# Optimization experiments

Hardware: AMD Instinct MI355X
Metric: run time of the kernel (lower is better)

## Reference

```python
import jax, jax.numpy as jnp
import numpy as np


def setup_inputs() -> dict:
    key = jax.random.key(0)
    k1, k2, k3 = jax.random.split(key, 3)
    B, T, D, H = 64, 512, 1024, 1024
    x = jax.random.normal(k1, (B, T, D), dtype=jnp.float32)
    state = jnp.zeros((B, H), dtype=jnp.float32)
    W = jax.random.normal(k2, (H, H), dtype=jnp.float32) / np.sqrt(H).astype(np.float32)
    U = jax.random.normal(k3, (D, H), dtype=jnp.float32) / np.sqrt(D).astype(np.float32)
    b = jnp.zeros((H,), dtype=jnp.float32)
    return {"x": x, "state": state, "W": W, "U": U, "b": b}


def reference(x, state, W, U, b):
    # x: (B, T, D) -> precompute input projection for all steps: (T, B, H)
    xU = jnp.einsum('btd,dh->tbh', x, U) + b

    def step(h, xu_t):
        h = jnp.tanh(xu_t + h @ W)
        return h, h

    final_state, outs = jax.lax.scan(step, state, xU)  # outs: (T, B, H)
    outs = jnp.transpose(outs, (1, 0, 2))  # (B, T, H)
    return outs, final_state
```

## Files before the change

kernel.cpp:

```cpp
#include <hip/hip_runtime.h>
#include <hip/hip_fp16.h>

typedef float  f4v __attribute__((ext_vector_type(4)));
typedef _Float16 h8v __attribute__((ext_vector_type(8)));
typedef _Float16 h4v __attribute__((ext_vector_type(4)));

#define B_ 64
#define T_ 512
#define H_ 1024

__global__ __launch_bounds__(256) void k_transpose_cvt(const float* __restrict__ src,
                                                       _Float16* __restrict__ dst) {
  __shared__ _Float16 tile[64][72];
  int r0 = blockIdx.y * 64, c0 = blockIdx.x * 64;
  int t = threadIdx.x;
  for (int i = 0; i < 4; ++i) {
    int r = i * 16 + (t >> 4);
    int c = (t & 15) * 4;
    f4v v = *reinterpret_cast<const f4v*>(src + (long)(r0 + r) * 1024 + c0 + c);
    tile[c + 0][r] = (_Float16)v.x;
    tile[c + 1][r] = (_Float16)v.y;
    tile[c + 2][r] = (_Float16)v.z;
    tile[c + 3][r] = (_Float16)v.w;
  }
  __syncthreads();
  for (int i = 0; i < 2; ++i) {
    int rr = i * 32 + (t >> 3);
    int cc = (t & 7) * 8;
    *reinterpret_cast<h8v*>(dst + (long)(c0 + rr) * 1024 + r0 + cc) =
        *reinterpret_cast<const h8v*>(&tile[rr][cc]);
  }
}

#define SWZG(r, kh) ((((r) * 64) + ((kh) * 2)) ^ (((r) & 3) << 4))

__global__ __launch_bounds__(256) void k_gemm_xu(const float* __restrict__ x,
                                                 const _Float16* __restrict__ Ut,
                                                 const float* __restrict__ bias,
                                                 float* __restrict__ out) {
  __shared__ __attribute__((aligned(16))) unsigned char Asm[128 * 32 * 2];
  __shared__ __attribute__((aligned(16))) unsigned char Bsm[128 * 32 * 2];
  int bid = blockIdx.x;
  int nt = bid & 7, mt = bid >> 3;
  int t = threadIdx.x;
  int row = t >> 1, kc = (t & 1) * 16;
  long gA = (long)(mt * 128 + row) * 1024 + kc;
  long gB = (long)(nt * 128 + row) * 1024 + kc;
  int wid = t >> 6, lane = t & 63;
  int wr = (wid >> 1) * 64, wc = (wid & 1) * 64;
  int l15 = lane & 15, khi = (lane >> 4) * 8;

  f4v acc[4][4];
  for (int i = 0; i < 4; ++i)
    for (int j = 0; j < 4; ++j) acc[i][j] = (f4v){0.f, 0.f, 0.f, 0.f};

  f4v ra[4];
  h8v rb[2];
  {
    const float* ap = x + gA;
    ra[0] = *(const f4v*)(ap);     ra[1] = *(const f4v*)(ap + 4);
    ra[2] = *(const f4v*)(ap + 8); ra[3] = *(const f4v*)(ap + 12);
    const _Float16* bp = Ut + gB;
    rb[0] = *(const h8v*)(bp);     rb[1] = *(const h8v*)(bp + 8);
  }
  for (int kt = 0; kt < 32; ++kt) {
    h8v ah0, ah1;
    for (int j = 0; j < 4; ++j) {
      ah0[j]     = (_Float16)ra[0][j];
      ah0[j + 4] = (_Float16)ra[1][j];
      ah1[j]     = (_Float16)ra[2][j];
      ah1[j + 4] = (_Float16)ra[3][j];
    }
    *(h8v*)(Asm + SWZG(row, kc))     = ah0;
    *(h8v*)(Asm + SWZG(row, kc + 8)) = ah1;
    *(h8v*)(Bsm + SWZG(row, kc))     = rb[0];
    *(h8v*)(Bsm + SWZG(row, kc + 8)) = rb[1];
    __syncthreads();
    if (kt < 31) {
      const float* ap = x + gA + (kt + 1) * 32;
      ra[0] = *(const f4v*)(ap);     ra[1] = *(const f4v*)(ap + 4);
      ra[2] = *(const f4v*)(ap + 8); ra[3] = *(const f4v*)(ap + 12);
      const _Float16* bp = Ut + gB + (kt + 1) * 32;
      rb[0] = *(const h8v*)(bp);     rb[1] = *(const h8v*)(bp + 8);
    }
    h8v af[4], bf[4];
    for (int mi = 0; mi < 4; ++mi)
      af[mi] = *(const h8v*)(Asm + SWZG(wr + mi * 16 + l15, khi));
    for (int ni = 0; ni < 4; ++ni)
      bf[ni] = *(const h8v*)(Bsm + SWZG(wc + ni * 16 + l15, khi));
    for (int mi = 0; mi < 4; ++mi)
      for (int ni = 0; ni < 4; ++ni)
        acc[mi][ni] = __builtin_amdgcn_mfma_f32_16x16x32_f16(af[mi], bf[ni], acc[mi][ni], 0, 0, 0);
    __syncthreads();
  }
  int coff = nt * 128 + wc, roff = mt * 128 + wr;
  for (int ni = 0; ni < 4; ++ni) {
    int col = coff + ni * 16 + l15;
    float bb = bias[col];
    for (int mi = 0; mi < 4; ++mi) {
      int rbase = roff + mi * 16 + (lane >> 4) * 4;
      for (int j = 0; j < 4; ++j)
        out[(long)(rbase + j) * 1024 + col] = acc[mi][ni][j] + bb;
    }
  }
}

#define SWZS(r, kh) ((((r) * 2048) + ((kh) * 2)) ^ (((r) & 7) << 4))

__global__ __launch_bounds__(256) void k_scan(const float* __restrict__ state,
                                              float* __restrict__ out,
                                              const _Float16* __restrict__ Wt,
                                              unsigned int* __restrict__ ctr) {
  extern __shared__ __attribute__((aligned(16))) unsigned char smem[];
  unsigned char* Wl = smem;
  unsigned char* Hl = smem + 65536;
  int t = threadIdx.x;
  int cl = blockIdx.x & 7;
  int mm = blockIdx.x >> 3;

  {
    int r = t >> 3, c8 = t & 7;
    const _Float16* wsrc = Wt + (long)(mm * 32 + r) * 1024;
    for (int j = 0; j < 16; ++j) {
      int kh = (c8 + 8 * j) * 8;
      *(h8v*)(Wl + SWZS(r, kh)) = *(const h8v*)(wsrc + kh);
    }
  }

  unsigned int* myctr = ctr + cl * 64;
  int wid = t >> 6, lane = t & 63;
  int srow = t >> 5, slane = t & 31;
  long b = cl * 8 + srow;
  int l15 = lane & 15, khi8 = (lane >> 4) * 8;
  int arow = lane & 7;
  int bro = wid * 16 + l15;
  int hi = lane >> 4;
  int gcol = mm * 32 + wid * 16 + l15;

  for (int step = 0; step < T_; ++step) {
    const float* hsrc = (step == 0) ? (state + b * 1024)
                                    : (out + (b * T_ + (step - 1)) * 1024);
    const float* hp = hsrc + slane * 4;
    f4v w0, w1, w2, w3, w4, w5, w6, w7;
    asm volatile(
        "global_load_dwordx4 %0, %8, off sc0 sc1\n\t"
        "global_load_dwordx4 %1, %8, off offset:512 sc0 sc1\n\t"
        "global_load_dwordx4 %2, %8, off offset:1024 sc0 sc1\n\t"
        "global_load_dwordx4 %3, %8, off offset:1536 sc0 sc1\n\t"
        "global_load_dwordx4 %4, %8, off offset:2048 sc0 sc1\n\t"
        "global_load_dwordx4 %5, %8, off offset:2560 sc0 sc1\n\t"
        "global_load_dwordx4 %6, %8, off offset:3072 sc0 sc1\n\t"
        "global_load_dwordx4 %7, %8, off offset:3584 sc0 sc1\n\t"
        "s_waitcnt vmcnt(0)"
        : "=&v"(w0), "=&v"(w1), "=&v"(w2), "=&v"(w3),
          "=&v"(w4), "=&v"(w5), "=&v"(w6), "=&v"(w7)
        : "v"(hp)
        : "memory");
    {
      f4v wv[8] = {w0, w1, w2, w3, w4, w5, w6, w7};
#pragma unroll
      for (int j = 0; j < 8; ++j) {
        int k = (slane + 32 * j) * 4;
        h4v hv;
        hv[0] = (_Float16)wv[j][0]; hv[1] = (_Float16)wv[j][1];
        hv[2] = (_Float16)wv[j][2]; hv[3] = (_Float16)wv[j][3];
        *(h4v*)(Hl + SWZS(srow, k)) = hv;
      }
    }
    __syncthreads();

    if (wid < 2) {
      float xuv[4];
      long addr0 = 0;
      if (hi < 2) {
        addr0 = ((long)(cl * 8 + hi * 4) * T_ + step) * 1024 + gcol;
#pragma unroll
        for (int j = 0; j < 4; ++j) xuv[j] = out[addr0 + (long)j * T_ * 1024];
      }
      f4v acc0 = (f4v){0.f, 0.f, 0.f, 0.f}, acc1 = acc0;
#pragma unroll
      for (int s = 0; s < 32; s += 2) {
        int k0 = s * 32 + khi8, k1 = (s + 1) * 32 + khi8;
        h8v af0 = *(const h8v*)(Hl + SWZS(arow, k0));
        h8v bf0 = *(const h8v*)(Wl + SWZS(bro, k0));
        h8v af1 = *(const h8v*)(Hl + SWZS(arow, k1));
        h8v bf1 = *(const h8v*)(Wl + SWZS(bro, k1));
        acc0 = __builtin_amdgcn_mfma_f32_16x16x32_f16(af0, bf0, acc0, 0, 0, 0);
        acc1 = __builtin_amdgcn_mfma_f32_16x16x32_f16(af1, bf1, acc1, 0, 0, 0);
      }
      f4v acc = acc0 + acc1;
      if (hi < 2) {
        float v0 = tanhf(acc[0] + xuv[0]);
        float v1 = tanhf(acc[1] + xuv[1]);
        float v2 = tanhf(acc[2] + xuv[2]);
        float v3 = tanhf(acc[3] + xuv[3]);
        float* p0 = out + addr0;
        float* p1 = p0 + (long)T_ * 1024;
        float* p2 = p1 + (long)T_ * 1024;
        float* p3 = p2 + (long)T_ * 1024;
        asm volatile(
            "global_store_dword %0, %4, off sc0 sc1\n\t"
            "global_store_dword %1, %5, off sc0 sc1\n\t"
            "global_store_dword %2, %6, off sc0 sc1\n\t"
            "global_store_dword %3, %7, off sc0 sc1\n\t"
            "s_waitcnt vmcnt(0)"
            :: "v"(p0), "v"(p1), "v"(p2), "v"(p3),
               "v"(v0), "v"(v1), "v"(v2), "v"(v3)
            : "memory");
        if (step == T_ - 1) {
          long r = (long)cl * 8 + hi * 4;
          float* q = out + (long)B_ * T_ * 1024 + r * 1024 + gcol;
          q[0] = v0; q[1024] = v1; q[2048] = v2; q[3072] = v3;
        }
      }
    }

    __syncthreads();
    if (t == 0) {
      __hip_atomic_fetch_add(myctr, 1u, __ATOMIC_RELAXED, __HIP_MEMORY_SCOPE_AGENT);
      unsigned int tgt = 32u * (unsigned)(step + 1);
      while (__hip_atomic_load(myctr, __ATOMIC_RELAXED, __HIP_MEMORY_SCOPE_AGENT) < tgt)
        __builtin_amdgcn_s_sleep(1);
    }
    __syncthreads();
  }
}

extern "C" void kernel_launch(void* const* d_in, const int* in_sizes, int n_in,
                              void* d_out, int out_size, void* d_ws, size_t ws_size,
                              hipStream_t stream) {
  const float* x     = (const float*)d_in[0];
  const float* state = (const float*)d_in[1];
  const float* W     = (const float*)d_in[2];
  const float* U     = (const float*)d_in[3];
  const float* bias  = (const float*)d_in[4];
  float* out = (float*)d_out;
  unsigned char* ws = (unsigned char*)d_ws;

  _Float16* Ut = (_Float16*)ws;
  _Float16* Wt = (_Float16*)(ws + (1u << 21));
  unsigned int* ctr = (unsigned int*)(ws + (1u << 22));

  hipMemsetAsync(ctr, 0, 8 * 64 * sizeof(unsigned int), stream);

  k_transpose_cvt<<<dim3(16, 16), 256, 0, stream>>>(U, Ut);
  k_transpose_cvt<<<dim3(16, 16), 256, 0, stream>>>(W, Wt);
  k_gemm_xu<<<2048, 256, 0, stream>>>(x, Ut, bias, out);

  hipFuncSetAttribute((const void*)k_scan, hipFuncAttributeMaxDynamicSharedMemorySize, 81920);
  void* args[] = {(void*)&state, (void*)&out, (void*)&Wt, (void*)&ctr};
  hipLaunchCooperativeKernel((void*)k_scan, dim3(256), dim3(256), args, 81920, stream);
}
```

Measured before the change: 1.602 ms.

## Replace counter barrier with step-tagged fp16 hidden-state exchange buffer

Removes the per-step atomic counter barrier and its two block-wide syncs. Each block now publishes the new hidden state as fp16 values packed with a 16-bit step tag into a double-buffered exchange array, and consumers spin-load until every tag matches the expected step. The shared-memory H buffer is double-buffered and the MFMA loop uses four accumulators instead of two. The exchange buffer reuses the Ut workspace after the projection GEMM and is reset with a 0xFF memset. Correctness depends on tag polling and cross-block visibility of the stores, and rows that arrive late are re-polled in full.

```diff
diff --git a/kernel.cpp b/kernel.cpp
--- a/kernel.cpp
+++ b/kernel.cpp
@@ -4,6 +4,7 @@
 typedef float  f4v __attribute__((ext_vector_type(4)));
 typedef _Float16 h8v __attribute__((ext_vector_type(8)));
 typedef _Float16 h4v __attribute__((ext_vector_type(4)));
+typedef unsigned uv4 __attribute__((ext_vector_type(4)));
 
 #define B_ 64
 #define T_ 512
@@ -107,16 +108,30 @@
 
 #define SWZS(r, kh) ((((r) * 2048) + ((kh) * 2)) ^ (((r) & 7) << 4))
 
+static __device__ __forceinline__ _Float16 lo_h(unsigned u) {
+  unsigned short s = (unsigned short)u;
+  _Float16 h;
+  __builtin_memcpy(&h, &s, 2);
+  return h;
+}
+static __device__ __forceinline__ unsigned pk(float f, unsigned tg) {
+  _Float16 h = (_Float16)f;
+  unsigned short s;
+  __builtin_memcpy(&s, &h, 2);
+  return (tg << 16) | (unsigned)s;
+}
+
 __global__ __launch_bounds__(256) void k_scan(const float* __restrict__ state,
                                               float* __restrict__ out,
                                               const _Float16* __restrict__ Wt,
-                                              unsigned int* __restrict__ ctr) {
+                                              unsigned* __restrict__ hx) {
   extern __shared__ __attribute__((aligned(16))) unsigned char smem[];
   unsigned char* Wl = smem;
-  unsigned char* Hl = smem + 65536;
+  unsigned char* Hl0 = smem + 65536;
   int t = threadIdx.x;
-  int cl = blockIdx.x & 7;
-  int mm = blockIdx.x >> 3;
+  int bid = blockIdx.x;
+  int cl = bid & 7;
+  int mm = bid >> 3;
 
   {
     int r = t >> 3, c8 = t & 7;
@@ -127,7 +142,6 @@
     }
   }
 
-  unsigned int* myctr = ctr + cl * 64;
   int wid = t >> 6, lane = t & 63;
   int srow = t >> 5, slane = t & 31;
   long b = cl * 8 + srow;
@@ -138,33 +152,64 @@
   int gcol = mm * 32 + wid * 16 + l15;
 
   for (int step = 0; step < T_; ++step) {
-    const float* hsrc = (step == 0) ? (state + b * 1024)
-                                    : (out + (b * T_ + (step - 1)) * 1024);
-    const float* hp = hsrc + slane * 4;
-    f4v w0, w1, w2, w3, w4, w5, w6, w7;
-    asm volatile(
-        "global_load_dwordx4 %0, %8, off sc0 sc1\n\t"
-        "global_load_dwordx4 %1, %8, off offset:512 sc0 sc1\n\t"
-        "global_load_dwordx4 %2, %8, off offset:1024 sc0 sc1\n\t"
-        "global_load_dwordx4 %3, %8, off offset:1536 sc0 sc1\n\t"
-        "global_load_dwordx4 %4, %8, off offset:2048 sc0 sc1\n\t"
-        "global_load_dwordx4 %5, %8, off offset:2560 sc0 sc1\n\t"
-        "global_load_dwordx4 %6, %8, off offset:3072 sc0 sc1\n\t"
-        "global_load_dwordx4 %7, %8, off offset:3584 sc0 sc1\n\t"
-        "s_waitcnt vmcnt(0)"
-        : "=&v"(w0), "=&v"(w1), "=&v"(w2), "=&v"(w3),
-          "=&v"(w4), "=&v"(w5), "=&v"(w6), "=&v"(w7)
-        : "v"(hp)
-        : "memory");
-    {
-      f4v wv[8] = {w0, w1, w2, w3, w4, w5, w6, w7};
+    unsigned char* Hb = Hl0 + (step & 1) * 16384;
+    if (step == 0) {
+      const float* hp0 = state + b * 1024 + slane * 4;
 #pragma unroll
       for (int j = 0; j < 8; ++j) {
-        int k = (slane + 32 * j) * 4;
-        h4v hv;
-        hv[0] = (_Float16)wv[j][0]; hv[1] = (_Float16)wv[j][1];
-        hv[2] = (_Float16)wv[j][2]; hv[3] = (_Float16)wv[j][3];
-        *(h4v*)(Hl + SWZS(srow, k)) = hv;
+        f4v v = *(const f4v*)(hp0 + 128 * j);
+        h4v hv = {(_Float16)v.x, (_Float16)v.y, (_Float16)v.z, (_Float16)v.w};
+        *(h4v*)(Hb + SWZS(srow, (slane + 32 * j) * 4)) = hv;
+      }
+    } else {
+      const unsigned* hp = hx + (((step - 1) & 1) * 64 + b) * 1024 + slane * 4;
+      unsigned tg = (unsigned)(step - 1);
+      uv4 c0;
+      for (;;) {
+        asm volatile("global_load_dwordx4 %0, %1, off sc0 sc1\n\ts_waitcnt vmcnt(0)"
+                     : "=v"(c0) : "v"(hp) : "memory");
+        if ((c0.x >> 16) == tg && (c0.y >> 16) == tg &&
+            (c0.z >> 16) == tg && (c0.w >> 16) == tg)
+          break;
+      }
+      uv4 c1, c2, c3, c4, c5, c6, c7;
+      for (;;) {
+        asm volatile(
+            "global_load_dwordx4 %0, %7, off offset:512 sc0 sc1\n\t"
+            "global_load_dwordx4 %1, %7, off offset:1024 sc0 sc1\n\t"
+            "global_load_dwordx4 %2, %7, off offset:1536 sc0 sc1\n\t"
+            "global_load_dwordx4 %3, %7, off offset:2048 sc0 sc1\n\t"
+            "global_load_dwordx4 %4, %7, off offset:2560 sc0 sc1\n\t"
+            "global_load_dwordx4 %5, %7, off offset:3072 sc0 sc1\n\t"
+            "global_load_dwordx4 %6, %7, off offset:3584 sc0 sc1\n\t"
+            "s_waitcnt vmcnt(0)"
+            : "=&v"(c1), "=&v"(c2), "=&v"(c3), "=&v"(c4),
+              "=&v"(c5), "=&v"(c6), "=&v"(c7)
+            : "v"(hp)
+            : "memory");
+        unsigned m = (c1.x >> 16) | (c1.y >> 16) | (c1.z >> 16) | (c1.w >> 16) |
+                     (c2.x >> 16) | (c2.y >> 16) | (c2.z >> 16) | (c2.w >> 16) |
+                     (c3.x >> 16) | (c3.y >> 16) | (c3.z >> 16) | (c3.w >> 16) |
+                     (c4.x >> 16) | (c4.y >> 16) | (c4.z >> 16) | (c4.w >> 16) |
+                     (c5.x >> 16) | (c5.y >> 16) | (c5.z >> 16) | (c5.w >> 16) |
+                     (c6.x >> 16) | (c6.y >> 16) | (c6.z >> 16) | (c6.w >> 16) |
+                     (c7.x >> 16) | (c7.y >> 16) | (c7.z >> 16) | (c7.w >> 16);
+        unsigned a = (c1.x >> 16) & (c1.y >> 16) & (c1.z >> 16) & (c1.w >> 16) &
+                     (c2.x >> 16) & (c2.y >> 16) & (c2.z >> 16) & (c2.w >> 16) &
+                     (c3.x >> 16) & (c3.y >> 16) & (c3.z >> 16) & (c3.w >> 16) &
+                     (c4.x >> 16) & (c4.y >> 16) & (c4.z >> 16) & (c4.w >> 16) &
+                     (c5.x >> 16) & (c5.y >> 16) & (c5.z >> 16) & (c5.w >> 16) &
+                     (c6.x >> 16) & (c6.y >> 16) & (c6.z >> 16) & (c6.w >> 16) &
+                     (c7.x >> 16) & (c7.y >> 16) & (c7.z >> 16) & (c7.w >> 16);
+        if (m == tg && a == tg) break;
+      }
+      {
+        uv4 cc[8] = {c0, c1, c2, c3, c4, c5, c6, c7};
+#pragma unroll
+        for (int j = 0; j < 8; ++j) {
+          h4v hv = {lo_h(cc[j].x), lo_h(cc[j].y), lo_h(cc[j].z), lo_h(cc[j].w)};
+          *(h4v*)(Hb + SWZS(srow, (slane + 32 * j) * 4)) = hv;
+        }
       }
     }
     __syncthreads();
@@ -177,36 +222,50 @@
 #pragma unroll
         for (int j = 0; j < 4; ++j) xuv[j] = out[addr0 + (long)j * T_ * 1024];
       }
-      f4v acc0 = (f4v){0.f, 0.f, 0.f, 0.f}, acc1 = acc0;
+      f4v ac0 = (f4v){0.f, 0.f, 0.f, 0.f}, ac1 = ac0, ac2 = ac0, ac3 = ac0;
 #pragma unroll
-      for (int s = 0; s < 32; s += 2) {
-        int k0 = s * 32 + khi8, k1 = (s + 1) * 32 + khi8;
-        h8v af0 = *(const h8v*)(Hl + SWZS(arow, k0));
+      for (int s = 0; s < 32; s += 4) {
+        int k0 = s * 32 + khi8, k1 = k0 + 32, k2 = k0 + 64, k3 = k0 + 96;
+        h8v af0 = *(const h8v*)(Hb + SWZS(arow, k0));
         h8v bf0 = *(const h8v*)(Wl + SWZS(bro, k0));
-        h8v af1 = *(const h8v*)(Hl + SWZS(arow, k1));
+        h8v af1 = *(const h8v*)(Hb + SWZS(arow, k1));
         h8v bf1 = *(const h8v*)(Wl + SWZS(bro, k1));
-        acc0 = __builtin_amdgcn_mfma_f32_16x16x32_f16(af0, bf0, acc0, 0, 0, 0);
-        acc1 = __builtin_amdgcn_mfma_f32_16x16x32_f16(af1, bf1, acc1, 0, 0, 0);
-      }
-      f4v acc = acc0 + acc1;
+        h8v af2 = *(const h8v*)(Hb + SWZS(arow, k2));
+        h8v bf2 = *(const h8v*)(Wl + SWZS(bro, k2));
+        h8v af3 = *(const h8v*)(Hb + SWZS(arow, k3));
+        h8v bf3 = *(const h8v*)(Wl + SWZS(bro, k3));
+        ac0 = __builtin_amdgcn_mfma_f32_16x16x32_f16(af0, bf0, ac0, 0, 0, 0);
+        ac1 = __builtin_amdgcn_mfma_f32_16x16x32_f16(af1, bf1, ac1, 0, 0, 0);
+        ac2 = __builtin_amdgcn_mfma_f32_16x16x32_f16(af2, bf2, ac2, 0, 0, 0);
+        ac3 = __builtin_amdgcn_mfma_f32_16x16x32_f16(af3, bf3, ac3, 0, 0, 0);
+      }
+      f4v acc = (ac0 + ac1) + (ac2 + ac3);
       if (hi < 2) {
         float v0 = tanhf(acc[0] + xuv[0]);
         float v1 = tanhf(acc[1] + xuv[1]);
         float v2 = tanhf(acc[2] + xuv[2]);
         float v3 = tanhf(acc[3] + xuv[3]);
-        float* p0 = out + addr0;
-        float* p1 = p0 + (long)T_ * 1024;
-        float* p2 = p1 + (long)T_ * 1024;
-        float* p3 = p2 + (long)T_ * 1024;
-        asm volatile(
-            "global_store_dword %0, %4, off sc0 sc1\n\t"
-            "global_store_dword %1, %5, off sc0 sc1\n\t"
-            "global_store_dword %2, %6, off sc0 sc1\n\t"
-            "global_store_dword %3, %7, off sc0 sc1\n\t"
-            "s_waitcnt vmcnt(0)"
-            :: "v"(p0), "v"(p1), "v"(p2), "v"(p3),
-               "v"(v0), "v"(v1), "v"(v2), "v"(v3)
-            : "memory");
+        if (step < T_ - 1) {
+          unsigned u0 = pk(v0, (unsigned)step), u1 = pk(v1, (unsigned)step);
+          unsigned u2 = pk(v2, (unsigned)step), u3 = pk(v3, (unsigned)step);
+          unsigned* q0 = hx + ((long)(step & 1) * 64 + cl * 8 + hi * 4) * 1024 + gcol;
+          unsigned* q1 = q0 + 1024;
+          unsigned* q2 = q0 + 2048;
+          unsigned* q3 = q0 + 3072;
+          asm volatile(
+              "global_store_dword %0, %4, off sc0 sc1\n\t"
+              "global_store_dword %1, %5, off sc0 sc1\n\t"
+              "global_store_dword %2, %6, off sc0 sc1\n\t"
+              "global_store_dword %3, %7, off sc0 sc1\n\t"
+              "s_waitcnt vmcnt(0)"
+              :: "v"(q0), "v"(q1), "v"(q2), "v"(q3),
+                 "v"(u0), "v"(u1), "v"(u2), "v"(u3)
+              : "memory");
+        }
+        out[addr0]                      = v0;
+        out[addr0 + (long)T_ * 1024]    = v1;
+        out[addr0 + (long)T_ * 2048]    = v2;
+        out[addr0 + (long)T_ * 3072]    = v3;
         if (step == T_ - 1) {
           long r = (long)cl * 8 + hi * 4;
           float* q = out + (long)B_ * T_ * 1024 + r * 1024 + gcol;
@@ -214,15 +273,6 @@
         }
       }
     }
-
-    __syncthreads();
-    if (t == 0) {
-      __hip_atomic_fetch_add(myctr, 1u, __ATOMIC_RELAXED, __HIP_MEMORY_SCOPE_AGENT);
-      unsigned int tgt = 32u * (unsigned)(step + 1);
-      while (__hip_atomic_load(myctr, __ATOMIC_RELAXED, __HIP_MEMORY_SCOPE_AGENT) < tgt)
-        __builtin_amdgcn_s_sleep(1);
-    }
-    __syncthreads();
   }
 }
 
@@ -239,15 +289,15 @@
 
   _Float16* Ut = (_Float16*)ws;
   _Float16* Wt = (_Float16*)(ws + (1u << 21));
-  unsigned int* ctr = (unsigned int*)(ws + (1u << 22));
-
-  hipMemsetAsync(ctr, 0, 8 * 64 * sizeof(unsigned int), stream);
+  unsigned* hx = (unsigned*)ws;
 
   k_transpose_cvt<<<dim3(16, 16), 256, 0, stream>>>(U, Ut);
   k_transpose_cvt<<<dim3(16, 16), 256, 0, stream>>>(W, Wt);
   k_gemm_xu<<<2048, 256, 0, stream>>>(x, Ut, bias, out);
 
-  hipFuncSetAttribute((const void*)k_scan, hipFuncAttributeMaxDynamicSharedMemorySize, 81920);
-  void* args[] = {(void*)&state, (void*)&out, (void*)&Wt, (void*)&ctr};
-  hipLaunchCooperativeKernel((void*)k_scan, dim3(256), dim3(256), args, 81920, stream);
-}
+  hipMemsetAsync(hx, 0xFF, 2u * 64u * 1024u * 4u, stream);
+
+  hipFuncSetAttribute((const void*)k_scan, hipFuncAttributeMaxDynamicSharedMemorySize, 98304);
+  void* args[] = {(void*)&state, (void*)&out, (void*)&Wt, (void*)&hx};
+  hipLaunchCooperativeKernel((void*)k_scan, dim3(256), dim3(256), args, 98304, stream);
+}
```

After: 2.099 ms. +31.0%, slower.

## Rework scan step barrier with double-buffered hidden state and runtime fast-path detection

Applied to the files above, without the earlier changes.

The scan now double-buffers the hidden-state tile in LDS, and each block writes its own freshly computed fp16 outputs directly into the next buffer. It also drops one of the two per-step __syncthreads and moves the wait to the start of the next step, so the xU prefetch overlaps with it. A startup probe checks whether the 32 blocks of a cluster share an L2 atomic domain; if so, a fast mode uses non-bypassing loads and stores, skips reloading its own columns, and polls the counter with atomic adds instead of sleeping. This aims to cut per-step barrier latency and coherent-memory traffic, at the risk of subtle memory-ordering bugs on the fast path.

```diff
diff --git a/kernel.cpp b/kernel.cpp
--- a/kernel.cpp
+++ b/kernel.cpp
@@ -110,13 +110,19 @@
 __global__ __launch_bounds__(256) void k_scan(const float* __restrict__ state,
                                               float* __restrict__ out,
                                               const _Float16* __restrict__ Wt,
-                                              unsigned int* __restrict__ ctr) {
+                                              unsigned* __restrict__ ctr) {
   extern __shared__ __attribute__((aligned(16))) unsigned char smem[];
   unsigned char* Wl = smem;
-  unsigned char* Hl = smem + 65536;
+  unsigned char* Hl0 = smem + 65536;
+  __shared__ int fastflag;
   int t = threadIdx.x;
-  int cl = blockIdx.x & 7;
-  int mm = blockIdx.x >> 3;
+  int bid = blockIdx.x;
+  int cl = bid & 7;
+  int mm = bid >> 3;
+
+  unsigned* stepc = ctr + cl * 32;
+  unsigned* testc = ctr + 256 + cl * 32;
+  unsigned* gbar  = ctr + 512;
 
   {
     int r = t >> 3, c8 = t & 7;
@@ -127,7 +133,20 @@
     }
   }
 
-  unsigned int* myctr = ctr + cl * 64;
+  if (t == 0) {
+    unsigned one = 1u, zero = 0u, got;
+    asm volatile("global_atomic_add %0, %1, off\n\ts_waitcnt vmcnt(0)"
+                 :: "v"(testc), "v"(one) : "memory");
+    __hip_atomic_fetch_add(gbar, 1u, __ATOMIC_RELAXED, __HIP_MEMORY_SCOPE_AGENT);
+    while (__hip_atomic_load(gbar, __ATOMIC_RELAXED, __HIP_MEMORY_SCOPE_AGENT) < 256u)
+      __builtin_amdgcn_s_sleep(2);
+    asm volatile("global_atomic_add %0, %1, %2, off sc0\n\ts_waitcnt vmcnt(0)"
+                 : "=&v"(got) : "v"(testc), "v"(zero) : "memory");
+    fastflag = (got == 32u);
+  }
+  __syncthreads();
+  const bool fastm = (fastflag != 0);
+
   int wid = t >> 6, lane = t & 63;
   int srow = t >> 5, slane = t & 31;
   long b = cl * 8 + srow;
@@ -136,59 +155,101 @@
   int bro = wid * 16 + l15;
   int hi = lane >> 4;
   int gcol = mm * 32 + wid * 16 + l15;
+  bool prod = (wid < 2) && (hi < 2);
 
   for (int step = 0; step < T_; ++step) {
-    const float* hsrc = (step == 0) ? (state + b * 1024)
-                                    : (out + (b * T_ + (step - 1)) * 1024);
-    const float* hp = hsrc + slane * 4;
-    f4v w0, w1, w2, w3, w4, w5, w6, w7;
-    asm volatile(
-        "global_load_dwordx4 %0, %8, off sc0 sc1\n\t"
-        "global_load_dwordx4 %1, %8, off offset:512 sc0 sc1\n\t"
-        "global_load_dwordx4 %2, %8, off offset:1024 sc0 sc1\n\t"
-        "global_load_dwordx4 %3, %8, off offset:1536 sc0 sc1\n\t"
-        "global_load_dwordx4 %4, %8, off offset:2048 sc0 sc1\n\t"
-        "global_load_dwordx4 %5, %8, off offset:2560 sc0 sc1\n\t"
-        "global_load_dwordx4 %6, %8, off offset:3072 sc0 sc1\n\t"
-        "global_load_dwordx4 %7, %8, off offset:3584 sc0 sc1\n\t"
-        "s_waitcnt vmcnt(0)"
-        : "=&v"(w0), "=&v"(w1), "=&v"(w2), "=&v"(w3),
-          "=&v"(w4), "=&v"(w5), "=&v"(w6), "=&v"(w7)
-        : "v"(hp)
-        : "memory");
-    {
-      f4v wv[8] = {w0, w1, w2, w3, w4, w5, w6, w7};
+    unsigned char* Hb = Hl0 + (step & 1) * 16384;
+
+    float xuv[4];
+    long addr0 = 0;
+    if (prod) {
+      addr0 = ((long)(cl * 8 + hi * 4) * T_ + step) * 1024 + gcol;
+#pragma unroll
+      for (int j = 0; j < 4; ++j) xuv[j] = out[addr0 + (long)j * T_ * 1024];
+    }
+
+    if (step == 0) {
+      const float* hp0 = state + b * 1024 + slane * 4;
 #pragma unroll
       for (int j = 0; j < 8; ++j) {
-        int k = (slane + 32 * j) * 4;
-        h4v hv;
-        hv[0] = (_Float16)wv[j][0]; hv[1] = (_Float16)wv[j][1];
-        hv[2] = (_Float16)wv[j][2]; hv[3] = (_Float16)wv[j][3];
-        *(h4v*)(Hl + SWZS(srow, k)) = hv;
+        f4v v = *(const f4v*)(hp0 + 128 * j);
+        h4v hv = {(_Float16)v.x, (_Float16)v.y, (_Float16)v.z, (_Float16)v.w};
+        *(h4v*)(Hb + SWZS(srow, (slane + 32 * j) * 4)) = hv;
+      }
+    } else {
+      if (t == 0) {
+        unsigned tgt = 32u * (unsigned)step;
+        if (fastm) {
+          unsigned cur, zero = 0u;
+          do {
+            asm volatile("global_atomic_add %0, %1, %2, off sc0\n\ts_waitcnt vmcnt(0)"
+                         : "=&v"(cur) : "v"(stepc), "v"(zero) : "memory");
+          } while (cur < tgt);
+        } else {
+          while (__hip_atomic_load(stepc, __ATOMIC_RELAXED, __HIP_MEMORY_SCOPE_AGENT) < tgt)
+            __builtin_amdgcn_s_sleep(1);
+        }
+      }
+      __syncthreads();
+
+      const float* hrow = out + (b * T_ + (step - 1)) * 1024;
+      if (fastm) {
+#pragma unroll
+        for (int j = 0; j < 8; ++j) {
+          int c0 = (slane + 32 * j) * 4;
+          if ((c0 >> 5) == mm) continue;
+          f4v v = *(const f4v*)(hrow + c0);
+          h4v hv = {(_Float16)v.x, (_Float16)v.y, (_Float16)v.z, (_Float16)v.w};
+          *(h4v*)(Hb + SWZS(srow, c0)) = hv;
+        }
+      } else {
+        const float* hp = hrow + slane * 4;
+        f4v w0, w1, w2, w3, w4, w5, w6, w7;
+        asm volatile(
+            "global_load_dwordx4 %0, %8, off sc0 sc1\n\t"
+            "global_load_dwordx4 %1, %8, off offset:512 sc0 sc1\n\t"
+            "global_load_dwordx4 %2, %8, off offset:1024 sc0 sc1\n\t"
+            "global_load_dwordx4 %3, %8, off offset:1536 sc0 sc1\n\t"
+            "global_load_dwordx4 %4, %8, off offset:2048 sc0 sc1\n\t"
+            "global_load_dwordx4 %5, %8, off offset:2560 sc0 sc1\n\t"
+            "global_load_dwordx4 %6, %8, off offset:3072 sc0 sc1\n\t"
+            "global_load_dwordx4 %7, %8, off offset:3584 sc0 sc1\n\t"
+            "s_waitcnt vmcnt(0)"
+            : "=&v"(w0), "=&v"(w1), "=&v"(w2), "=&v"(w3),
+              "=&v"(w4), "=&v"(w5), "=&v"(w6), "=&v"(w7)
+            : "v"(hp)
+            : "memory");
+        f4v wv[8] = {w0, w1, w2, w3, w4, w5, w6, w7};
+#pragma unroll
+        for (int j = 0; j < 8; ++j) {
+          int c0 = (slane + 32 * j) * 4;
+          h4v hv = {(_Float16)wv[j][0], (_Float16)wv[j][1],
+                    (_Float16)wv[j][2], (_Float16)wv[j][3]};
+          *(h4v*)(Hb + SWZS(srow, c0)) = hv;
+        }
       }
     }
     __syncthreads();
 
     if (wid < 2) {
-      float xuv[4];
-      long addr0 = 0;
-      if (hi < 2) {
-        addr0 = ((long)(cl * 8 + hi * 4) * T_ + step) * 1024 + gcol;
-#pragma unroll
-        for (int j = 0; j < 4; ++j) xuv[j] = out[addr0 + (long)j * T_ * 1024];
-      }
-      f4v acc0 = (f4v){0.f, 0.f, 0.f, 0.f}, acc1 = acc0;
-#pragma unroll
-      for (int s = 0; s < 32; s += 2) {
-        int k0 = s * 32 + khi8, k1 = (s + 1) * 32 + khi8;
-        h8v af0 = *(const h8v*)(Hl + SWZS(arow, k0));
+      f4v ac0 = (f4v){0.f, 0.f, 0.f, 0.f}, ac1 = ac0, ac2 = ac0, ac3 = ac0;
+#pragma unroll
+      for (int s = 0; s < 32; s += 4) {
+        int k0 = s * 32 + khi8, k1 = k0 + 32, k2 = k0 + 64, k3 = k0 + 96;
+        h8v af0 = *(const h8v*)(Hb + SWZS(arow, k0));
         h8v bf0 = *(const h8v*)(Wl + SWZS(bro, k0));
-        h8v af1 = *(const h8v*)(Hl + SWZS(arow, k1));
+        h8v af1 = *(const h8v*)(Hb + SWZS(arow, k1));
         h8v bf1 = *(const h8v*)(Wl + SWZS(bro, k1));
-        acc0 = __builtin_amdgcn_mfma_f32_16x16x32_f16(af0, bf0, acc0, 0, 0, 0);
-        acc1 = __builtin_amdgcn_mfma_f32_16x16x32_f16(af1, bf1, acc1, 0, 0, 0);
-      }
-      f4v acc = acc0 + acc1;
+        h8v af2 = *(const h8v*)(Hb + SWZS(arow, k2));
+        h8v bf2 = *(const h8v*)(Wl + SWZS(bro, k2));
+        h8v af3 = *(const h8v*)(Hb + SWZS(arow, k3));
+        h8v bf3 = *(const h8v*)(Wl + SWZS(bro, k3));
+        ac0 = __builtin_amdgcn_mfma_f32_16x16x32_f16(af0, bf0, ac0, 0, 0, 0);
+        ac1 = __builtin_amdgcn_mfma_f32_16x16x32_f16(af1, bf1, ac1, 0, 0, 0);
+        ac2 = __builtin_amdgcn_mfma_f32_16x16x32_f16(af2, bf2, ac2, 0, 0, 0);
+        ac3 = __builtin_amdgcn_mfma_f32_16x16x32_f16(af3, bf3, ac3, 0, 0, 0);
+      }
+      f4v acc = (ac0 + ac1) + (ac2 + ac3);
       if (hi < 2) {
         float v0 = tanhf(acc[0] + xuv[0]);
         float v1 = tanhf(acc[1] + xuv[1]);
@@ -198,15 +259,28 @@
         float* p1 = p0 + (long)T_ * 1024;
         float* p2 = p1 + (long)T_ * 1024;
         float* p3 = p2 + (long)T_ * 1024;
-        asm volatile(
-            "global_store_dword %0, %4, off sc0 sc1\n\t"
-            "global_store_dword %1, %5, off sc0 sc1\n\t"
-            "global_store_dword %2, %6, off sc0 sc1\n\t"
-            "global_store_dword %3, %7, off sc0 sc1\n\t"
-            "s_waitcnt vmcnt(0)"
-            :: "v"(p0), "v"(p1), "v"(p2), "v"(p3),
-               "v"(v0), "v"(v1), "v"(v2), "v"(v3)
-            : "memory");
+        if (fastm) {
+          p0[0] = v0; p1[0] = v1; p2[0] = v2; p3[0] = v3;
+        } else {
+          asm volatile(
+              "global_store_dword %0, %4, off sc0 sc1\n\t"
+              "global_store_dword %1, %5, off sc0 sc1\n\t"
+              "global_store_dword %2, %6, off sc0 sc1\n\t"
+              "global_store_dword %3, %7, off sc0 sc1\n\t"
+              "s_waitcnt vmcnt(0)"
+              :: "v"(p0), "v"(p1), "v"(p2), "v"(p3),
+                 "v"(v0), "v"(v1), "v"(v2), "v"(v3)
+              : "memory");
+        }
+        if (step < T_ - 1) {
+          unsigned char* Hn = Hl0 + ((step + 1) & 1) * 16384;
+          int cb = gcol & ~3, co = (gcol & 3) * 2;
+          int r0r = hi * 4;
+          *(_Float16*)(Hn + SWZS(r0r + 0, cb) + co) = (_Float16)v0;
+          *(_Float16*)(Hn + SWZS(r0r + 1, cb) + co) = (_Float16)v1;
+          *(_Float16*)(Hn + SWZS(r0r + 2, cb) + co) = (_Float16)v2;
+          *(_Float16*)(Hn + SWZS(r0r + 3, cb) + co) = (_Float16)v3;
+        }
         if (step == T_ - 1) {
           long r = (long)cl * 8 + hi * 4;
           float* q = out + (long)B_ * T_ * 1024 + r * 1024 + gcol;
@@ -215,14 +289,18 @@
       }
     }
 
+    if (prod) {
+      asm volatile("s_waitcnt vmcnt(0)" ::: "memory");
+    }
     __syncthreads();
     if (t == 0) {
-      __hip_atomic_fetch_add(myctr, 1u, __ATOMIC_RELAXED, __HIP_MEMORY_SCOPE_AGENT);
-      unsigned int tgt = 32u * (unsigned)(step + 1);
-      while (__hip_atomic_load(myctr, __ATOMIC_RELAXED, __HIP_MEMORY_SCOPE_AGENT) < tgt)
-        __builtin_amdgcn_s_sleep(1);
-    }
-    __syncthreads();
+      if (fastm) {
+        unsigned one = 1u;
+        asm volatile("global_atomic_add %0, %1, off" :: "v"(stepc), "v"(one) : "memory");
+      } else {
+        __hip_atomic_fetch_add(stepc, 1u, __ATOMIC_RELAXED, __HIP_MEMORY_SCOPE_AGENT);
+      }
+    }
   }
 }
 
@@ -239,15 +317,15 @@
 
   _Float16* Ut = (_Float16*)ws;
   _Float16* Wt = (_Float16*)(ws + (1u << 21));
-  unsigned int* ctr = (unsigned int*)(ws + (1u << 22));
-
-  hipMemsetAsync(ctr, 0, 8 * 64 * sizeof(unsigned int), stream);
+  unsigned* ctr = (unsigned*)(ws + (1u << 22));
+
+  hipMemsetAsync(ctr, 0, 4096, stream);
 
   k_transpose_cvt<<<dim3(16, 16), 256, 0, stream>>>(U, Ut);
   k_transpose_cvt<<<dim3(16, 16), 256, 0, stream>>>(W, Wt);
   k_gemm_xu<<<2048, 256, 0, stream>>>(x, Ut, bias, out);
 
-  hipFuncSetAttribute((const void*)k_scan, hipFuncAttributeMaxDynamicSharedMemorySize, 81920);
+  hipFuncSetAttribute((const void*)k_scan, hipFuncAttributeMaxDynamicSharedMemorySize, 98304);
   void* args[] = {(void*)&state, (void*)&out, (void*)&Wt, (void*)&ctr};
-  hipLaunchCooperativeKernel((void*)k_scan, dim3(256), dim3(256), args, 81920, stream);
+  hipLaunchCooperativeKernel((void*)k_scan, dim3(256), dim3(256), args, 98304, stream);
 }
```

Measured after the change: 1.880 ms. +17.3%, slower.
